# Optimization experiments

Hardware: AMD Instinct MI355X
Metric: run time of the kernel (lower is better)

The kernel has to match this reference:

```python
import jax, jax.numpy as jnp
import numpy as np

BUCKETS = 64
DIM = 512  # self.dim, used only for attention scaling


def setup_inputs() -> dict:
    key = jax.random.key(0)
    k1, k2, k3, k4 = jax.random.split(key, 4)
    b, h, t, dh = 4, 8, 8192, 64
    q = jax.random.normal(k1, (b, h, t, dh), dtype=jnp.float32)
    k = jax.random.normal(k2, (b, h, t, dh), dtype=jnp.float32)
    v = jax.random.normal(k3, (b, h, t, dh), dtype=jnp.float32)
    W = jax.random.normal(k4, (1, h, 2 * dh, BUCKETS), dtype=jnp.float32)  # SimpleSortNet.linear
    return {"q": q, "k": k, "v": v, "W": W}


def reference(q, k, v, W):
    b, h, t, dh = q.shape
    bh = b * h
    bsz = t // BUCKETS  # bucket size = 128

    # merge batch and heads, then bucket: [bh, buckets, bsz, dh]
    b_q = q.reshape(bh, BUCKETS, bsz, dh)
    b_k = k.reshape(bh, BUCKETS, bsz, dh)
    b_v = v.reshape(bh, BUCKETS, bsz, dh)

    # --- SimpleSortNet (non_permutative=True -> softmax, no gumbel) ---
    # summarize each bucket by sum over tokens, concat q/k summaries
    x = jnp.concatenate([b_q.sum(axis=2), b_k.sum(axis=2)], axis=-1)  # [bh, buckets, 2*dh]
    Wb = jnp.broadcast_to(W, (b, h, 2 * dh, BUCKETS)).reshape(bh, 2 * dh, BUCKETS)
    R = jax.nn.relu(jnp.einsum('bud,bdv->buv', x, Wb))  # [bh, buckets, buckets]
    R = jax.nn.softmax(R, axis=-1)

    # zero_all_but_top: keep only top-1 entry along last dim (dim=2)
    top_idx = jnp.argmax(R, axis=-1)  # [bh, buckets]
    top_mask = jnp.arange(BUCKETS) == top_idx[..., None]
    R = jnp.where(top_mask, R, jnp.zeros((), dtype=R.dtype))

    # reorder key/value buckets by (sparsified) R
    b_k_r = jnp.einsum('buv,bvtd->butd', R, b_k)
    b_v_r = jnp.einsum('buv,bvtd->butd', R, b_v)

    # buckets == kv_buckets: attend over [reordered bucket ; own bucket]
    bk = jnp.concatenate([b_k_r, b_k], axis=2)  # [bh, buckets, 2*bsz, dh]
    bv = jnp.concatenate([b_v_r, b_v], axis=2)

    # bucketed attention; note: original scales by self.dim ** -0.5 (full dim)
    dots = jnp.einsum('buie,buje->buij', b_q, bk) * (DIM ** -0.5)
    attn = jax.nn.softmax(dots, axis=-1)
    out = jnp.einsum('buij,buje->buie', attn, bv)  # [bh, buckets, bsz, dh]

    return out.reshape(b, h, t, dh)
```

## Files before the change

kernel.cpp:

```cpp
#include <hip/hip_runtime.h>


#define T_TOK 8192
#define CQ (0.04419417382415922f * 1.4426950408889634f)
#define FIXED_M 12.0f

#define KB_OFF 0
#define VT_OFF 16384
#define XB_OFF 32768
#define QP_OFF 33280
#define KP_OFF 34304

typedef __attribute__((ext_vector_type(16))) float f32x16;
typedef __attribute__((ext_vector_type(8))) short bf16x8;

__device__ __forceinline__ unsigned cvtpk(float lo, float hi) {
  unsigned r;
  asm("v_cvt_pk_bf16_f32 %0, %1, %2" : "=v"(r) : "v"(lo), "v"(hi));
  return r;
}
__device__ __forceinline__ float exp2v(float x) {
  float r;
  asm("v_exp_f32 %0, %1\n\ts_nop 0" : "=v"(r) : "v"(x));
  return r;
}

#define ATTN_TILE(TLOC, VUHALF)                                                \
  {                                                                            \
    int tokr = (TLOC) * 32 + ln;                                               \
    f32x16 acc;                                                                \
    _Pragma("unroll") for (int r = 0; r < 16; ++r) acc[r] = 0.f;               \
    _Pragma("unroll") for (int sl = 0; sl < 4; ++sl) {                         \
      int addr =                                                               \
          KB_OFF + tokr * 128 + ((sl * 32 + lhi * 16) ^ ((tokr & 7) << 4));    \
      bf16x8 af = *reinterpret_cast<const bf16x8*>(smem + addr);               \
      acc = __builtin_amdgcn_mfma_f32_32x32x16_bf16(af, qf[sl], acc, 0, 0, 0); \
    }                                                                          \
    _Pragma("unroll") for (int r = 0; r < 16; ++r) {                           \
      float lg = (VUHALF) ? acc[r] * ru : acc[r];                              \
      float p = exp2v(lg - FIXED_M);                                           \
      acc[r] = p;                                                              \
      lsum += p;                                                               \
    }                                                                          \
    _Pragma("unroll") for (int ks = 0; ks < 2; ++ks) {                         \
      int r0 = 8 * ks;                                                         \
      unsigned aA, bA, aB, bB;                                                 \
      asm("v_cvt_pk_bf16_f32 %0, %1, %2"                                       \
          : "=v"(aA) : "v"(acc[r0 + 0]), "v"(acc[r0 + 1]));                    \
      asm("v_cvt_pk_bf16_f32 %0, %1, %2"                                       \
          : "=v"(bA) : "v"(acc[r0 + 2]), "v"(acc[r0 + 3]));                    \
      asm("v_cvt_pk_bf16_f32 %0, %1, %2"                                       \
          : "=v"(aB) : "v"(acc[r0 + 4]), "v"(acc[r0 + 5]));                    \
      asm("v_cvt_pk_bf16_f32 %0, %1, %2"                                       \
          : "=v"(bB) : "v"(acc[r0 + 6]), "v"(acc[r0 + 7]));                    \
      asm("s_nop 1\n\tv_permlane32_swap_b32 %0, %1\n\ts_nop 1"                 \
          : "+v"(aA), "+v"(aB));                                               \
      asm("s_nop 1\n\tv_permlane32_swap_b32 %0, %1\n\ts_nop 1"                 \
          : "+v"(bA), "+v"(bB));                                               \
      union { unsigned uu[4]; bf16x8 f; } pf;                                  \
      pf.uu[0] = aA; pf.uu[1] = bA; pf.uu[2] = aB; pf.uu[3] = bB;              \
      int t2 = 2 * ((TLOC) * 32 + ks * 16 + lhi * 8);                          \
      {                                                                        \
        int d = ln;                                                            \
        int addr = VT_OFF + d * 256 + (t2 ^ ((d & 15) << 4));                  \
        bf16x8 vf = *reinterpret_cast<const bf16x8*>(smem + addr);             \
        o0 = __builtin_amdgcn_mfma_f32_32x32x16_bf16(pf.f, vf, o0, 0, 0, 0);   \
      }                                                                        \
      {                                                                        \
        int d = 32 + ln;                                                       \
        int addr = VT_OFF + d * 256 + (t2 ^ ((d & 15) << 4));                  \
        bf16x8 vf = *reinterpret_cast<const bf16x8*>(smem + addr);             \
        o1 = __builtin_amdgcn_mfma_f32_32x32x16_bf16(pf.f, vf, o1, 0, 0, 0);   \
      }                                                                        \
    }                                                                          \
  }

__global__ __launch_bounds__(256, 2) void k3_attn(
    const float* __restrict__ q, const float* __restrict__ k,
    const float* __restrict__ v, const float* __restrict__ W,
    float* __restrict__ out) {
  __shared__ unsigned char smem[38400];

  int L = blockIdx.x;
  int G = ((L & 7) << 8) | (L >> 3);
  int bhi = G >> 6, u = G & 63;
  int tid = threadIdx.x;
  int l = tid & 63;
  int w = tid >> 6;
  int lhi = l >> 5;
  int ln = l & 31;
  int hh = bhi & 7;

  const float* kb = k + (size_t)bhi * (T_TOK * 64);
  const float* vb = v + (size_t)bhi * (T_TOK * 64);
  int c4 = tid & 15;
  int tp = tid >> 2;

  const float* qrow = q + ((size_t)bhi * T_TOK + (size_t)u * 128 + w * 32 + ln) * 64;
  float4 qld[8];
  #pragma unroll
  for (int sl = 0; sl < 4; ++sl) {
    qld[2 * sl] = *reinterpret_cast<const float4*>(qrow + sl * 16 + lhi * 8);
    qld[2 * sl + 1] = *reinterpret_cast<const float4*>(qrow + sl * 16 + lhi * 8 + 4);
  }
  float4 kld[8];
  #pragma unroll
  for (int it = 0; it < 8; ++it) {
    int row = (tid >> 4) + it * 16;
    kld[it] = *reinterpret_cast<const float4*>(
        kb + (size_t)(u * 128 + row) * 64 + c4 * 4);
  }
  float4 vld[8];
  {
    const float* s0 = vb + ((size_t)(u * 128 + 2 * tp)) * 64 + (tid & 3) * 4;
    #pragma unroll
    for (int i = 0; i < 4; ++i) {
      vld[i] = *reinterpret_cast<const float4*>(s0 + i * 16);
      vld[4 + i] = *reinterpret_cast<const float4*>(s0 + i * 16 + 64);
    }
  }

  bf16x8 qf[4];
  float qs[32];
  #pragma unroll
  for (int sl = 0; sl < 4; ++sl) {
    float4 a4 = qld[2 * sl], b4 = qld[2 * sl + 1];
    qs[sl * 8 + 0] = a4.x; qs[sl * 8 + 1] = a4.y;
    qs[sl * 8 + 2] = a4.z; qs[sl * 8 + 3] = a4.w;
    qs[sl * 8 + 4] = b4.x; qs[sl * 8 + 5] = b4.y;
    qs[sl * 8 + 6] = b4.z; qs[sl * 8 + 7] = b4.w;
    union { unsigned uu[4]; bf16x8 f; } qu;
    qu.uu[0] = cvtpk(a4.x * CQ, a4.y * CQ);
    qu.uu[1] = cvtpk(a4.z * CQ, a4.w * CQ);
    qu.uu[2] = cvtpk(b4.x * CQ, b4.y * CQ);
    qu.uu[3] = cvtpk(b4.z * CQ, b4.w * CQ);
    qf[sl] = qu.f;
  }
  #pragma unroll
  for (int off = 1; off < 32; off <<= 1) {
    #pragma unroll
    for (int j = 0; j < 32; ++j) qs[j] += __shfl_xor(qs[j], off, 64);
  }
  if (ln == 0) {
    float* qp = (float*)(smem + QP_OFF) + w * 64 + lhi * 8;
    #pragma unroll
    for (int sl = 0; sl < 4; ++sl) {
      #pragma unroll
      for (int j = 0; j < 8; ++j) qp[sl * 16 + j] = qs[sl * 8 + j];
    }
  }

  float4 ksum = make_float4(0.f, 0.f, 0.f, 0.f);
  #pragma unroll
  for (int it = 0; it < 8; ++it) {
    float4 val = kld[it];
    ksum.x += val.x; ksum.y += val.y; ksum.z += val.z; ksum.w += val.w;
    int row = (tid >> 4) + it * 16;
    int addr = KB_OFF + row * 128 + ((c4 * 8) ^ ((row & 7) << 4));
    *reinterpret_cast<uint2*>(smem + addr) =
        make_uint2(cvtpk(val.x, val.y), cvtpk(val.z, val.w));
  }
  *reinterpret_cast<float4*>(smem + KP_OFF + tid * 16) = ksum;

  #pragma unroll
  for (int i = 0; i < 4; ++i) {
    int dq = (tid & 3) + 4 * i;
    int t2 = 4 * tp;
    const float* fa = (const float*)&vld[i];
    const float* fc = (const float*)&vld[4 + i];
    #pragma unroll
    for (int jj = 0; jj < 4; ++jj) {
      int d = dq * 4 + jj;
      int addr = VT_OFF + d * 256 + (t2 ^ ((d & 15) << 4));
      *reinterpret_cast<unsigned*>(smem + addr) = cvtpk(fa[jj], fc[jj]);
    }
  }

  __syncthreads();

  if (tid < 128) {
    float* xbw = (float*)(smem + XB_OFF);
    if (tid < 64) {
      const float* qp = (const float*)(smem + QP_OFF);
      xbw[tid] = qp[tid] + qp[64 + tid] + qp[128 + tid] + qp[192 + tid];
    } else {
      int d = tid - 64;
      const float* kp = (const float*)(smem + KP_OFF);
      float xk = 0.f;
      #pragma unroll
      for (int g = 0; g < 16; ++g) xk += kp[(g * 16 + (d >> 2)) * 4 + (d & 3)];
      xbw[64 + d] = xk;
    }
  }
  __syncthreads();

  const float* xb = (const float*)(smem + XB_OFF);
  const float* wcol = W + (size_t)hh * 8192 + l;
  float a0 = 0.f, a1 = 0.f, a2 = 0.f, a3 = 0.f;
  #pragma unroll
  for (int kk = 0; kk < 128; kk += 4) {
    a0 = fmaf(xb[kk + 0], wcol[(size_t)(kk + 0) * 64], a0);
    a1 = fmaf(xb[kk + 1], wcol[(size_t)(kk + 1) * 64], a1);
    a2 = fmaf(xb[kk + 2], wcol[(size_t)(kk + 2) * 64], a2);
    a3 = fmaf(xb[kk + 3], wcol[(size_t)(kk + 3) * 64], a3);
  }
  float a = fmaxf((a0 + a1) + (a2 + a3), 0.f);
  float bvv = a; int bi = l;
  #pragma unroll
  for (int off = 1; off < 64; off <<= 1) {
    float ov = __shfl_xor(bvv, off, 64);
    int oi = __shfl_xor(bi, off, 64);
    if (ov > bvv || (ov == bvv && oi < bi)) { bvv = ov; bi = oi; }
  }
  float e = __expf(a - bvv);
  #pragma unroll
  for (int off = 1; off < 64; off <<= 1) e += __shfl_xor(e, off, 64);
  int vu = bi;
  float ru = 1.f / e;

  float4 kvu[8];
  #pragma unroll
  for (int it = 0; it < 8; ++it) {
    int row = (tid >> 4) + it * 16;
    kvu[it] = *reinterpret_cast<const float4*>(
        kb + (size_t)(vu * 128 + row) * 64 + c4 * 4);
  }
  float4 vvu[8];
  {
    const float* s0 = vb + ((size_t)(vu * 128 + 2 * tp)) * 64 + (tid & 3) * 4;
    #pragma unroll
    for (int i = 0; i < 4; ++i) {
      vvu[i] = *reinterpret_cast<const float4*>(s0 + i * 16);
      vvu[4 + i] = *reinterpret_cast<const float4*>(s0 + i * 16 + 64);
    }
  }

  f32x16 o0, o1;
  #pragma unroll
  for (int r = 0; r < 16; ++r) { o0[r] = 0.f; o1[r] = 0.f; }
  float lsum = 0.f;

  #pragma unroll
  for (int t8 = 0; t8 < 4; ++t8) ATTN_TILE(t8, false)

  __syncthreads();

  #pragma unroll
  for (int it = 0; it < 8; ++it) {
    int row = (tid >> 4) + it * 16;
    int addr = KB_OFF + row * 128 + ((c4 * 8) ^ ((row & 7) << 4));
    *reinterpret_cast<uint2*>(smem + addr) =
        make_uint2(cvtpk(kvu[it].x, kvu[it].y), cvtpk(kvu[it].z, kvu[it].w));
  }
  #pragma unroll
  for (int i = 0; i < 4; ++i) {
    int dq = (tid & 3) + 4 * i;
    int t2 = 4 * tp;
    const float* fa = (const float*)&vvu[i];
    const float* fc = (const float*)&vvu[4 + i];
    #pragma unroll
    for (int jj = 0; jj < 4; ++jj) {
      int d = dq * 4 + jj;
      int addr = VT_OFF + d * 256 + (t2 ^ ((d & 15) << 4));
      *reinterpret_cast<unsigned*>(smem + addr) = cvtpk(fa[jj] * ru, fc[jj] * ru);
    }
  }
  __syncthreads();

  #pragma unroll
  for (int t8 = 0; t8 < 4; ++t8) ATTN_TILE(t8, true)

  lsum += __shfl_xor(lsum, 32, 64);
  float inv = 1.f / lsum;
  float* ob = out + ((size_t)bhi * T_TOK + (size_t)u * 128 + w * 32) * 64;
  #pragma unroll
  for (int r = 0; r < 16; ++r) {
    int row = (r & 3) + 8 * (r >> 2) + 4 * lhi;
    float invr = __shfl(inv, row, 64);
    ob[(size_t)row * 64 + ln] = o0[r] * invr;
    ob[(size_t)row * 64 + 32 + ln] = o1[r] * invr;
  }
}

extern "C" void kernel_launch(void* const* d_in, const int* in_sizes, int n_in,
                              void* d_out, int out_size, void* d_ws, size_t ws_size,
                              hipStream_t stream) {
  const float* q = (const float*)d_in[0];
  const float* k = (const float*)d_in[1];
  const float* v = (const float*)d_in[2];
  const float* W = (const float*)d_in[3];
  float* out = (float*)d_out;

  hipLaunchKernelGGL(k3_attn, dim3(2048), dim3(256), 0, stream, q, k, v, W, out);
}
```

Baseline: 68.13 us.

## Process two buckets per block and prefetch next bucket during attention

Each block now handles two consecutive buckets, halving the grid to 1024 blocks. While the second attention half of the first bucket runs, the q/k/v loads for the second bucket are issued so their latency overlaps compute. This costs a serial dependency per block, fewer blocks for latency hiding across the GPU, and extra register pressure from holding the prefetched data alongside the accumulators.

```diff
diff --git a/kernel.cpp b/kernel.cpp
--- a/kernel.cpp
+++ b/kernel.cpp
@@ -24,6 +24,29 @@
   asm("v_exp_f32 %0, %1\n\ts_nop 0" : "=v"(r) : "v"(x));
   return r;
 }
+
+#define ISSUE_P0(U)                                                            \
+  {                                                                            \
+    const float* qrow_ =                                                       \
+        q + ((size_t)bhi * T_TOK + (size_t)(U) * 128 + w * 32 + ln) * 64;      \
+    _Pragma("unroll") for (int sl = 0; sl < 4; ++sl) {                         \
+      qld[2 * sl] =                                                            \
+          *reinterpret_cast<const float4*>(qrow_ + sl * 16 + lhi * 8);         \
+      qld[2 * sl + 1] =                                                        \
+          *reinterpret_cast<const float4*>(qrow_ + sl * 16 + lhi * 8 + 4);     \
+    }                                                                          \
+    _Pragma("unroll") for (int it = 0; it < 8; ++it) {                         \
+      int row = (tid >> 4) + it * 16;                                          \
+      kld[it] = *reinterpret_cast<const float4*>(                              \
+          kb + (size_t)((U) * 128 + row) * 64 + c4 * 4);                       \
+    }                                                                          \
+    const float* s0_ =                                                         \
+        vb + ((size_t)((U) * 128 + 2 * tp)) * 64 + (tid & 3) * 4;              \
+    _Pragma("unroll") for (int i = 0; i < 4; ++i) {                            \
+      vld[i] = *reinterpret_cast<const float4*>(s0_ + i * 16);                 \
+      vld[4 + i] = *reinterpret_cast<const float4*>(s0_ + i * 16 + 64);        \
+    }                                                                          \
+  }
 
 #define ATTN_TILE(TLOC, VUHALF)                                                \
   {                                                                            \
@@ -82,8 +105,9 @@
   __shared__ unsigned char smem[38400];
 
   int L = blockIdx.x;
-  int G = ((L & 7) << 8) | (L >> 3);
-  int bhi = G >> 6, u = G & 63;
+  int P = ((L & 7) << 7) | (L >> 3);
+  int bhi = P >> 5;
+  int u0 = (2 * P) & 63;
   int tid = threadIdx.x;
   int l = tid & 63;
   int w = tid >> 6;
@@ -96,189 +120,179 @@
   int c4 = tid & 15;
   int tp = tid >> 2;
 
-  const float* qrow = q + ((size_t)bhi * T_TOK + (size_t)u * 128 + w * 32 + ln) * 64;
-  float4 qld[8];
+  float4 qld[8], kld[8], vld[8];
+  ISSUE_P0(u0)
+
   #pragma unroll
-  for (int sl = 0; sl < 4; ++sl) {
-    qld[2 * sl] = *reinterpret_cast<const float4*>(qrow + sl * 16 + lhi * 8);
-    qld[2 * sl + 1] = *reinterpret_cast<const float4*>(qrow + sl * 16 + lhi * 8 + 4);
-  }
-  float4 kld[8];
-  #pragma unroll
-  for (int it = 0; it < 8; ++it) {
-    int row = (tid >> 4) + it * 16;
-    kld[it] = *reinterpret_cast<const float4*>(
-        kb + (size_t)(u * 128 + row) * 64 + c4 * 4);
-  }
-  float4 vld[8];
-  {
-    const float* s0 = vb + ((size_t)(u * 128 + 2 * tp)) * 64 + (tid & 3) * 4;
+  for (int bkt = 0; bkt < 2; ++bkt) {
+    int u = u0 + bkt;
+
+    bf16x8 qf[4];
+    float qs[32];
+    #pragma unroll
+    for (int sl = 0; sl < 4; ++sl) {
+      float4 a4 = qld[2 * sl], b4 = qld[2 * sl + 1];
+      qs[sl * 8 + 0] = a4.x; qs[sl * 8 + 1] = a4.y;
+      qs[sl * 8 + 2] = a4.z; qs[sl * 8 + 3] = a4.w;
+      qs[sl * 8 + 4] = b4.x; qs[sl * 8 + 5] = b4.y;
+      qs[sl * 8 + 6] = b4.z; qs[sl * 8 + 7] = b4.w;
+      union { unsigned uu[4]; bf16x8 f; } qu;
+      qu.uu[0] = cvtpk(a4.x * CQ, a4.y * CQ);
+      qu.uu[1] = cvtpk(a4.z * CQ, a4.w * CQ);
+      qu.uu[2] = cvtpk(b4.x * CQ, b4.y * CQ);
+      qu.uu[3] = cvtpk(b4.z * CQ, b4.w * CQ);
+      qf[sl] = qu.f;
+    }
+    #pragma unroll
+    for (int off = 1; off < 32; off <<= 1) {
+      #pragma unroll
+      for (int j = 0; j < 32; ++j) qs[j] += __shfl_xor(qs[j], off, 64);
+    }
+    if (ln == 0) {
+      float* qp = (float*)(smem + QP_OFF) + w * 64 + lhi * 8;
+      #pragma unroll
+      for (int sl = 0; sl < 4; ++sl) {
+        #pragma unroll
+        for (int j = 0; j < 8; ++j) qp[sl * 16 + j] = qs[sl * 8 + j];
+      }
+    }
+
+    float4 ksum = make_float4(0.f, 0.f, 0.f, 0.f);
+    #pragma unroll
+    for (int it = 0; it < 8; ++it) {
+      float4 val = kld[it];
+      ksum.x += val.x; ksum.y += val.y; ksum.z += val.z; ksum.w += val.w;
+      int row = (tid >> 4) + it * 16;
+      int addr = KB_OFF + row * 128 + ((c4 * 8) ^ ((row & 7) << 4));
+      *reinterpret_cast<uint2*>(smem + addr) =
+          make_uint2(cvtpk(val.x, val.y), cvtpk(val.z, val.w));
+    }
+    *reinterpret_cast<float4*>(smem + KP_OFF + tid * 16) = ksum;
+
     #pragma unroll
     for (int i = 0; i < 4; ++i) {
-      vld[i] = *reinterpret_cast<const float4*>(s0 + i * 16);
-      vld[4 + i] = *reinterpret_cast<const float4*>(s0 + i * 16 + 64);
-    }
-  }
-
-  bf16x8 qf[4];
-  float qs[32];
-  #pragma unroll
-  for (int sl = 0; sl < 4; ++sl) {
-    float4 a4 = qld[2 * sl], b4 = qld[2 * sl + 1];
-    qs[sl * 8 + 0] = a4.x; qs[sl * 8 + 1] = a4.y;
-    qs[sl * 8 + 2] = a4.z; qs[sl * 8 + 3] = a4.w;
-    qs[sl * 8 + 4] = b4.x; qs[sl * 8 + 5] = b4.y;
-    qs[sl * 8 + 6] = b4.z; qs[sl * 8 + 7] = b4.w;
-    union { unsigned uu[4]; bf16x8 f; } qu;
-    qu.uu[0] = cvtpk(a4.x * CQ, a4.y * CQ);
-    qu.uu[1] = cvtpk(a4.z * CQ, a4.w * CQ);
-    qu.uu[2] = cvtpk(b4.x * CQ, b4.y * CQ);
-    qu.uu[3] = cvtpk(b4.z * CQ, b4.w * CQ);
-    qf[sl] = qu.f;
-  }
-  #pragma unroll
-  for (int off = 1; off < 32; off <<= 1) {
-    #pragma unroll
-    for (int j = 0; j < 32; ++j) qs[j] += __shfl_xor(qs[j], off, 64);
-  }
-  if (ln == 0) {
-    float* qp = (float*)(smem + QP_OFF) + w * 64 + lhi * 8;
-    #pragma unroll
-    for (int sl = 0; sl < 4; ++sl) {
-      #pragma unroll
-      for (int j = 0; j < 8; ++j) qp[sl * 16 + j] = qs[sl * 8 + j];
-    }
-  }
-
-  float4 ksum = make_float4(0.f, 0.f, 0.f, 0.f);
-  #pragma unroll
-  for (int it = 0; it < 8; ++it) {
-    float4 val = kld[it];
-    ksum.x += val.x; ksum.y += val.y; ksum.z += val.z; ksum.w += val.w;
-    int row = (tid >> 4) + it * 16;
-    int addr = KB_OFF + row * 128 + ((c4 * 8) ^ ((row & 7) << 4));
-    *reinterpret_cast<uint2*>(smem + addr) =
-        make_uint2(cvtpk(val.x, val.y), cvtpk(val.z, val.w));
-  }
-  *reinterpret_cast<float4*>(smem + KP_OFF + tid * 16) = ksum;
-
-  #pragma unroll
-  for (int i = 0; i < 4; ++i) {
-    int dq = (tid & 3) + 4 * i;
-    int t2 = 4 * tp;
-    const float* fa = (const float*)&vld[i];
-    const float* fc = (const float*)&vld[4 + i];
-    #pragma unroll
-    for (int jj = 0; jj < 4; ++jj) {
-      int d = dq * 4 + jj;
-      int addr = VT_OFF + d * 256 + (t2 ^ ((d & 15) << 4));
-      *reinterpret_cast<unsigned*>(smem + addr) = cvtpk(fa[jj], fc[jj]);
-    }
-  }
-
-  __syncthreads();
-
-  if (tid < 128) {
-    float* xbw = (float*)(smem + XB_OFF);
-    if (tid < 64) {
-      const float* qp = (const float*)(smem + QP_OFF);
-      xbw[tid] = qp[tid] + qp[64 + tid] + qp[128 + tid] + qp[192 + tid];
-    } else {
-      int d = tid - 64;
-      const float* kp = (const float*)(smem + KP_OFF);
-      float xk = 0.f;
-      #pragma unroll
-      for (int g = 0; g < 16; ++g) xk += kp[(g * 16 + (d >> 2)) * 4 + (d & 3)];
-      xbw[64 + d] = xk;
-    }
-  }
-  __syncthreads();
-
-  const float* xb = (const float*)(smem + XB_OFF);
-  const float* wcol = W + (size_t)hh * 8192 + l;
-  float a0 = 0.f, a1 = 0.f, a2 = 0.f, a3 = 0.f;
-  #pragma unroll
-  for (int kk = 0; kk < 128; kk += 4) {
-    a0 = fmaf(xb[kk + 0], wcol[(size_t)(kk + 0) * 64], a0);
-    a1 = fmaf(xb[kk + 1], wcol[(size_t)(kk + 1) * 64], a1);
-    a2 = fmaf(xb[kk + 2], wcol[(size_t)(kk + 2) * 64], a2);
-    a3 = fmaf(xb[kk + 3], wcol[(size_t)(kk + 3) * 64], a3);
-  }
-  float a = fmaxf((a0 + a1) + (a2 + a3), 0.f);
-  float bvv = a; int bi = l;
-  #pragma unroll
-  for (int off = 1; off < 64; off <<= 1) {
-    float ov = __shfl_xor(bvv, off, 64);
-    int oi = __shfl_xor(bi, off, 64);
-    if (ov > bvv || (ov == bvv && oi < bi)) { bvv = ov; bi = oi; }
-  }
-  float e = __expf(a - bvv);
-  #pragma unroll
-  for (int off = 1; off < 64; off <<= 1) e += __shfl_xor(e, off, 64);
-  int vu = bi;
-  float ru = 1.f / e;
-
-  float4 kvu[8];
-  #pragma unroll
-  for (int it = 0; it < 8; ++it) {
-    int row = (tid >> 4) + it * 16;
-    kvu[it] = *reinterpret_cast<const float4*>(
-        kb + (size_t)(vu * 128 + row) * 64 + c4 * 4);
-  }
-  float4 vvu[8];
-  {
-    const float* s0 = vb + ((size_t)(vu * 128 + 2 * tp)) * 64 + (tid & 3) * 4;
+      int dq = (tid & 3) + 4 * i;
+      int t2 = 4 * tp;
+      const float* fa = (const float*)&vld[i];
+      const float* fc = (const float*)&vld[4 + i];
+      #pragma unroll
+      for (int jj = 0; jj < 4; ++jj) {
+        int d = dq * 4 + jj;
+        int addr = VT_OFF + d * 256 + (t2 ^ ((d & 15) << 4));
+        *reinterpret_cast<unsigned*>(smem + addr) = cvtpk(fa[jj], fc[jj]);
+      }
+    }
+
+    __syncthreads();
+
+    if (tid < 128) {
+      float* xbw = (float*)(smem + XB_OFF);
+      if (tid < 64) {
+        const float* qp = (const float*)(smem + QP_OFF);
+        xbw[tid] = qp[tid] + qp[64 + tid] + qp[128 + tid] + qp[192 + tid];
+      } else {
+        int d = tid - 64;
+        const float* kp = (const float*)(smem + KP_OFF);
+        float xk = 0.f;
+        #pragma unroll
+        for (int g = 0; g < 16; ++g)
+          xk += kp[(g * 16 + (d >> 2)) * 4 + (d & 3)];
+        xbw[64 + d] = xk;
+      }
+    }
+    __syncthreads();
+
+    const float* xb = (const float*)(smem + XB_OFF);
+    const float* wcol = W + (size_t)hh * 8192 + l;
+    float a0 = 0.f, a1 = 0.f, a2 = 0.f, a3 = 0.f;
+    #pragma unroll
+    for (int kk = 0; kk < 128; kk += 4) {
+      a0 = fmaf(xb[kk + 0], wcol[(size_t)(kk + 0) * 64], a0);
+      a1 = fmaf(xb[kk + 1], wcol[(size_t)(kk + 1) * 64], a1);
+      a2 = fmaf(xb[kk + 2], wcol[(size_t)(kk + 2) * 64], a2);
+      a3 = fmaf(xb[kk + 3], wcol[(size_t)(kk + 3) * 64], a3);
+    }
+    float a = fmaxf((a0 + a1) + (a2 + a3), 0.f);
+    float bvv = a; int bi = l;
+    #pragma unroll
+    for (int off = 1; off < 64; off <<= 1) {
+      float ov = __shfl_xor(bvv, off, 64);
+      int oi = __shfl_xor(bi, off, 64);
+      if (ov > bvv || (ov == bvv && oi < bi)) { bvv = ov; bi = oi; }
+    }
+    float e = __expf(a - bvv);
+    #pragma unroll
+    for (int off = 1; off < 64; off <<= 1) e += __shfl_xor(e, off, 64);
+    int vu = bi;
+    float ru = 1.f / e;
+
+    float4 kvu[8];
+    #pragma unroll
+    for (int it = 0; it < 8; ++it) {
+      int row = (tid >> 4) + it * 16;
+      kvu[it] = *reinterpret_cast<const float4*>(
+          kb + (size_t)(vu * 128 + row) * 64 + c4 * 4);
+    }
+    float4 vvu[8];
+    {
+      const float* s0 = vb + ((size_t)(vu * 128 + 2 * tp)) * 64 + (tid & 3) * 4;
+      #pragma unroll
+      for (int i = 0; i < 4; ++i) {
+        vvu[i] = *reinterpret_cast<const float4*>(s0 + i * 16);
+        vvu[4 + i] = *reinterpret_cast<const float4*>(s0 + i * 16 + 64);
+      }
+    }
+
+    f32x16 o0, o1;
+    #pragma unroll
+    for (int r = 0; r < 16; ++r) { o0[r] = 0.f; o1[r] = 0.f; }
+    float lsum = 0.f;
+
+    #pragma unroll
+    for (int t8 = 0; t8 < 4; ++t8) ATTN_TILE(t8, false)
+
+    __syncthreads();
+
+    #pragma unroll
+    for (int it = 0; it < 8; ++it) {
+      int row = (tid >> 4) + it * 16;
+      int addr = KB_OFF + row * 128 + ((c4 * 8) ^ ((row & 7) << 4));
+      *reinterpret_cast<uint2*>(smem + addr) =
+          make_uint2(cvtpk(kvu[it].x, kvu[it].y), cvtpk(kvu[it].z, kvu[it].w));
+    }
     #pragma unroll
     for (int i = 0; i < 4; ++i) {
-      vvu[i] = *reinterpret_cast<const float4*>(s0 + i * 16);
-      vvu[4 + i] = *reinterpret_cast<const float4*>(s0 + i * 16 + 64);
-    }
-  }
-
-  f32x16 o0, o1;
-  #pragma unroll
-  for (int r = 0; r < 16; ++r) { o0[r] = 0.f; o1[r] = 0.f; }
-  float lsum = 0.f;
-
-  #pragma unroll
-  for (int t8 = 0; t8 < 4; ++t8) ATTN_TILE(t8, false)
-
-  __syncthreads();
-
-  #pragma unroll
-  for (int it = 0; it < 8; ++it) {
-    int row = (tid >> 4) + it * 16;
-    int addr = KB_OFF + row * 128 + ((c4 * 8) ^ ((row & 7) << 4));
-    *reinterpret_cast<uint2*>(smem + addr) =
-        make_uint2(cvtpk(kvu[it].x, kvu[it].y), cvtpk(kvu[it].z, kvu[it].w));
-  }
-  #pragma unroll
-  for (int i = 0; i < 4; ++i) {
-    int dq = (tid & 3) + 4 * i;
-    int t2 = 4 * tp;
-    const float* fa = (const float*)&vvu[i];
-    const float* fc = (const float*)&vvu[4 + i];
-    #pragma unroll
-    for (int jj = 0; jj < 4; ++jj) {
-      int d = dq * 4 + jj;
-      int addr = VT_OFF + d * 256 + (t2 ^ ((d & 15) << 4));
-      *reinterpret_cast<unsigned*>(smem + addr) = cvtpk(fa[jj] * ru, fc[jj] * ru);
-    }
-  }
-  __syncthreads();
-
-  #pragma unroll
-  for (int t8 = 0; t8 < 4; ++t8) ATTN_TILE(t8, true)
-
-  lsum += __shfl_xor(lsum, 32, 64);
-  float inv = 1.f / lsum;
-  float* ob = out + ((size_t)bhi * T_TOK + (size_t)u * 128 + w * 32) * 64;
-  #pragma unroll
-  for (int r = 0; r < 16; ++r) {
-    int row = (r & 3) + 8 * (r >> 2) + 4 * lhi;
-    float invr = __shfl(inv, row, 64);
-    ob[(size_t)row * 64 + ln] = o0[r] * invr;
-    ob[(size_t)row * 64 + 32 + ln] = o1[r] * invr;
+      int dq = (tid & 3) + 4 * i;
+      int t2 = 4 * tp;
+      const float* fa = (const float*)&vvu[i];
+      const float* fc = (const float*)&vvu[4 + i];
+      #pragma unroll
+      for (int jj = 0; jj < 4; ++jj) {
+        int d = dq * 4 + jj;
+        int addr = VT_OFF + d * 256 + (t2 ^ ((d & 15) << 4));
+        *reinterpret_cast<unsigned*>(smem + addr) =
+            cvtpk(fa[jj] * ru, fc[jj] * ru);
+      }
+    }
+    __syncthreads();
+
+    if (bkt == 0) ISSUE_P0(u0 + 1)
+
+    #pragma unroll
+    for (int t8 = 0; t8 < 4; ++t8) ATTN_TILE(t8, true)
+
+    lsum += __shfl_xor(lsum, 32, 64);
+    float inv = 1.f / lsum;
+    float* ob = out + ((size_t)bhi * T_TOK + (size_t)u * 128 + w * 32) * 64;
+    #pragma unroll
+    for (int r = 0; r < 16; ++r) {
+      int row = (r & 3) + 8 * (r >> 2) + 4 * lhi;
+      float invr = __shfl(inv, row, 64);
+      ob[(size_t)row * 64 + ln] = o0[r] * invr;
+      ob[(size_t)row * 64 + 32 + ln] = o1[r] * invr;
+    }
+
+    if (bkt == 0) __syncthreads();
   }
 }
 
@@ -291,5 +305,5 @@
   const float* W = (const float*)d_in[3];
   float* out = (float*)d_out;
 
-  hipLaunchKernelGGL(k3_attn, dim3(2048), dim3(256), 0, stream, q, k, v, W, out);
+  hipLaunchKernelGGL(k3_attn, dim3(1024), dim3(256), 0, stream, q, k, v, W, out);
 }
```

After: 117.2 us. 72.0% more time.
